# Performance work log

Measured on AMD Instinct MI355X. Metric: run time of the kernel, lower is better.

The kernel has to match this reference:

```python
import jax, jax.numpy as jnp
import numpy as np
from jax import lax

N, E, D, L = 10000, 320000, 128, 5
ATOM_V, BOND_V, WHID, CHID, P = 128, 16, 64, 20, 10
BN_EPS = 1e-5


def setup_inputs() -> dict:
    key = jax.random.key(0)
    it = iter(jax.random.split(key, 40))

    def nrm(shape, fan_in):
        return jax.random.normal(next(it), shape, jnp.float32) / np.sqrt(fan_in).astype(np.float32)

    return {
        "x_feat": jax.random.randint(next(it), (N, 2), 0, ATOM_V),
        "edge_index": jax.random.randint(next(it), (2, E), 0, N),
        "edge_attr": jax.random.randint(next(it), (E, 3), 0, BOND_V),
        "norm_edge_weight": jax.random.uniform(next(it), (E,), jnp.float32),
        "norm_self_loop": jax.random.uniform(next(it), (N,), jnp.float32),
        "atom_emb": nrm((2, ATOM_V, D), 1.0),
        "curv_w1": nrm((D, CHID), D), "curv_b1": jnp.zeros((CHID,), jnp.float32),
        "curv_w2": nrm((CHID, 1), CHID), "curv_b2": jnp.zeros((1,), jnp.float32),
        "fn_w1": nrm((D, CHID), D), "fn_b1": jnp.zeros((CHID,), jnp.float32),
        "fn_w2": nrm((CHID, 1), CHID), "fn_b2": jnp.zeros((1,), jnp.float32),
        "wm_w1": nrm((E, WHID), E), "wm_b1": jnp.zeros((WHID,), jnp.float32),
        "wm_w2": nrm((WHID, WHID), WHID), "wm_b2": jnp.zeros((WHID,), jnp.float32),
        "wm_w3": nrm((WHID, E), WHID), "wm_b3": jnp.zeros((E,), jnp.float32),
        "bond_emb": nrm((L, 3, BOND_V, D), 1.0),
        "conv_w1": nrm((L, D, D), D), "conv_b1": jnp.zeros((L, D), jnp.float32),
        "conv_bn_g": jnp.ones((L, D), jnp.float32), "conv_bn_b": jnp.zeros((L, D), jnp.float32),
        "conv_w2": nrm((L, D, D), D), "conv_b2": jnp.zeros((L, D), jnp.float32),
        "conv_eps": jnp.full((L,), 0.1, jnp.float32),
        "bn_g": jnp.ones((L, D), jnp.float32), "bn_b": jnp.zeros((L, D), jnp.float32),
        "batch": jnp.zeros((N,), jnp.int32),
    }


def _forward(x_feat, edge_index, edge_attr, norm_edge_weight, norm_self_loop,
             atom_emb, curv_w1, curv_b1, curv_w2, curv_b2,
             fn_w1, fn_b1, fn_w2, fn_b2,
             wm_w1, wm_b1, wm_w2, wm_b2, wm_w3, wm_b3,
             bond_emb, conv_w1, conv_b1, conv_bn_g, conv_bn_b, conv_w2, conv_b2,
             conv_eps, bn_g, bn_b):
    relu, sig = jax.nn.relu, jax.nn.sigmoid
    src, dst = edge_index[0], edge_index[1]

    # AtomEncoder: sum of per-column embeddings -> [N, D]
    x = atom_emb[0][x_feat[:, 0]] + atom_emb[1][x_feat[:, 1]]

    # CurvatureMLP: sigmoid(MLP(x)) -> kappa [N, 1]
    kappa = sig(relu(x @ curv_w1 + curv_b1) @ curv_w2 + curv_b2)

    # WeightMLP over 1-D edge-feature-sum vector (single sample of dim E)
    ea = edge_attr.sum(axis=1).astype(jnp.float32)  # [E]
    w = relu(ea @ wm_w1 + wm_b1)
    w = relu(w @ wm_w2 + wm_b2)
    weights = sig(w @ wm_w3 + wm_b3)  # [E]

    # curvature terms: scatter_add at SRC (as in original compute_gamma*)
    seg = lambda v: jax.ops.segment_sum(v, src, num_segments=N)
    f = sig(relu(x @ fn_w1 + fn_b1) @ fn_w2 + fn_b2)[:, 0]  # [N]
    fd = f[dst] - f[src]
    gamma = 0.5 * seg(weights * fd * fd)              # [N]
    delta_f = seg(weights * fd)                       # [N]
    delta_gamma = seg(weights * (gamma[dst] - gamma[src]))
    gfd = 0.5 * seg(weights * fd * (delta_f[dst] - delta_f[src]))
    gamma2 = 0.5 * delta_gamma - gfd                  # [N]
    # NOTE: kappa [N,1] * gamma [N] broadcasts to [N,N] (faithful to original)
    curv_loss = jnp.sum(relu(kappa * gamma - gamma2)) - jnp.sum(kappa)

    kap = kappa[:, 0]

    def bn(h, g, b):  # BatchNorm1d in training mode (batch stats, biased var)
        m = h.mean(axis=0)
        v = jnp.var(h, axis=0)
        return g * (h - m) * lax.rsqrt(v + BN_EPS) + b

    h_list = [x]
    for l in range(L):
        k = min(int(N * P * l / 100), 100)  # num vertices to suppress
        if k > 0:
            idx = lax.top_k(kap, k)[1]
            vm = jnp.ones(N, jnp.float32).at[idx].set(0.0)
            mew = jnp.where((vm[src] == 0) | (vm[dst] == 0), 1e-5, 1.0)
        else:
            mew = jnp.ones(E, jnp.float32)
        # BondEncoder for this layer
        ee = (bond_emb[l, 0][edge_attr[:, 0]]
              + bond_emb[l, 1][edge_attr[:, 1]]
              + bond_emb[l, 2][edge_attr[:, 2]])  # [E, D]
        # message: norm2 * norm * relu(x_j + edge_emb); aggregate add at dst
        msg = (mew * norm_edge_weight)[:, None] * relu(h_list[l][src] + ee)
        aggr = jax.ops.segment_sum(msg, dst, num_segments=N)
        h = conv_eps[l] * norm_self_loop[:, None] * h_list[l] + aggr
        # conv MLP: Linear -> BN -> ReLU -> Linear
        h = relu(bn(h @ conv_w1[l] + conv_b1[l], conv_bn_g[l], conv_bn_b[l])) @ conv_w2[l] + conv_b2[l]
        h = bn(h, bn_g[l], bn_b[l])
        if l < L - 1:  # dropout has ratio 0.0 -> no-op
            h = relu(h)
        h_list.append(h)

    node_rep = h_list[0]
    for h in h_list[1:]:
        node_rep = node_rep + h
    return node_rep, curv_loss


def reference(x_feat, edge_index, edge_attr, norm_edge_weight, norm_self_loop,
              atom_emb, curv_w1, curv_b1, curv_w2, curv_b2,
              fn_w1, fn_b1, fn_w2, fn_b2,
              wm_w1, wm_b1, wm_w2, wm_b2, wm_w3, wm_b3,
              bond_emb, conv_w1, conv_b1, conv_bn_g, conv_bn_b, conv_w2, conv_b2,
              conv_eps, bn_g, bn_b, batch):
    return _forward(x_feat, edge_index, edge_attr, norm_edge_weight, norm_self_loop,
                    atom_emb, curv_w1, curv_b1, curv_w2, curv_b2,
                    fn_w1, fn_b1, fn_w2, fn_b2,
                    wm_w1, wm_b1, wm_w2, wm_b2, wm_w3, wm_b3,
                    bond_emb, conv_w1, conv_b1, conv_bn_g, conv_bn_b, conv_w2, conv_b2,
                    conv_eps, bn_g, bn_b)
```

## Files before the change

kernel.cpp:

```cpp
#include <hip/hip_runtime.h>
#include <hip/hip_bf16.h>
#include <math.h>

#define N_NODES 10000
#define N_EDGES 320000
#define DIM     128
#define NLAYERS 5
#define CHIDN   20
#define BNEPS   1e-5f
#define TOPK    100

__device__ __forceinline__ float sigmoidf_(float x){ return 1.0f/(1.0f + expf(-x)); }

__global__ __launch_bounds__(256) void k_node(
  const int* __restrict__ xf, const float* __restrict__ atom_emb,
  const float* __restrict__ cw1, const float* __restrict__ cb1,
  const float* __restrict__ cw2, const float* __restrict__ cb2,
  const float* __restrict__ fw1, const float* __restrict__ fb1,
  const float* __restrict__ fw2, const float* __restrict__ fb2,
  float* __restrict__ x_out, float* __restrict__ kap, float* __restrict__ fv,
  float* __restrict__ kapparts,
  int* __restrict__ counts, float* __restrict__ gamma, float* __restrict__ delta_f,
  float* __restrict__ dg, float* __restrict__ gfd, double* __restrict__ wh_acc)
{
  __shared__ float scw1[DIM*CHIDN];
  __shared__ float sfw1[DIM*CHIDN];
  __shared__ float sx[4][DIM];
  __shared__ float sred[4][64];
  int tid = threadIdx.x;
  if (tid < 4) {
    int n = blockIdx.x*4 + tid;
    counts[n]=0; gamma[n]=0.f; delta_f[n]=0.f; dg[n]=0.f; gfd[n]=0.f;
  }
  if (blockIdx.x == 0 && tid < 64) wh_acc[tid] = 0.0;
  for (int i=tid;i<DIM*CHIDN;i+=256){ scw1[i]=cw1[i]; sfw1[i]=fw1[i]; }
  int wid = tid>>6, lane = tid&63;
  int n = blockIdx.x*4 + wid;
  const float* e0 = atom_emb;
  const float* e1 = atom_emb + 128*DIM;
  int f0 = xf[n*2+0], f1 = xf[n*2+1];
  float2 a = *(const float2*)(e0 + f0*DIM + lane*2);
  float2 b = *(const float2*)(e1 + f1*DIM + lane*2);
  float2 xv; xv.x = a.x+b.x; xv.y = a.y+b.y;
  *(float2*)(x_out + (size_t)n*DIM + lane*2) = xv;
  sx[wid][lane*2] = xv.x; sx[wid][lane*2+1] = xv.y;
  __syncthreads();
  if (lane < CHIDN) {
    float acc = cb1[lane];
    for (int d=0; d<DIM; ++d) acc = fmaf(sx[wid][d], scw1[d*CHIDN+lane], acc);
    sred[wid][lane] = fmaxf(acc, 0.f) * cw2[lane];
  } else if (lane >= 32 && lane < 32+CHIDN) {
    int hh = lane-32;
    float acc = fb1[hh];
    for (int d=0; d<DIM; ++d) acc = fmaf(sx[wid][d], sfw1[d*CHIDN+hh], acc);
    sred[wid][32+hh] = fmaxf(acc, 0.f) * fw2[hh];
  }
  __syncthreads();
  if (lane == 0) {
    float s = cb2[0];
    for (int h=0;h<CHIDN;++h) s += sred[wid][h];
    float kp = sigmoidf_(s);
    kap[n] = kp;
    sred[wid][62] = kp;
  } else if (lane == 1) {
    float s = fb2[0];
    for (int h=0;h<CHIDN;++h) s += sred[wid][32+h];
    fv[n] = sigmoidf_(s);
  }
  __syncthreads();
  if (tid == 0) {
    kapparts[blockIdx.x] = sred[0][62] + sred[1][62] + sred[2][62] + sred[3][62];
  }
}

__global__ __launch_bounds__(256) void k_edge_pre(
  const int* __restrict__ ei, const int* __restrict__ eattr,
  const float* __restrict__ w1, int* __restrict__ counts, int* __restrict__ rank,
  double* __restrict__ wh_acc)
{
  __shared__ float part_[4][64];
  int tid = threadIdx.x;
  int wid = tid>>6, lane = tid&63;
  int bb = blockIdx.x*4 + wid;
  int e = bb*64 + lane;
  int a0=eattr[e*3], a1=eattr[e*3+1], a2=eattr[e*3+2];
  float ea = (float)(a0+a1+a2);
  int dst = ei[N_EDGES+e];
  rank[e] = atomicAdd(&counts[dst], 1);
  const float4* wrow = (const float4*)(w1 + (size_t)bb*64*64);
  int rsub = lane>>4, c4 = lane&15;
  float4 acc; acc.x=0.f; acc.y=0.f; acc.z=0.f; acc.w=0.f;
  #pragma unroll
  for (int i=0;i<16;++i) {
    float4 v = wrow[(i*4+rsub)*16 + c4];
    float eat = __shfl(ea, i*4+rsub);
    acc.x = fmaf(eat, v.x, acc.x);
    acc.y = fmaf(eat, v.y, acc.y);
    acc.z = fmaf(eat, v.z, acc.z);
    acc.w = fmaf(eat, v.w, acc.w);
  }
  acc.x += __shfl_xor(acc.x, 16); acc.y += __shfl_xor(acc.y, 16);
  acc.z += __shfl_xor(acc.z, 16); acc.w += __shfl_xor(acc.w, 16);
  acc.x += __shfl_xor(acc.x, 32); acc.y += __shfl_xor(acc.y, 32);
  acc.z += __shfl_xor(acc.z, 32); acc.w += __shfl_xor(acc.w, 32);
  if (lane < 16) ((float4*)part_[wid])[c4] = acc;
  __syncthreads();
  if (tid < 64) {
    float s = part_[0][tid]+part_[1][tid]+part_[2][tid]+part_[3][tid];
    atomicAdd(&wh_acc[tid], (double)s);
  }
}

__global__ __launch_bounds__(1024) void k_topk_scan(
  const float* __restrict__ kap, int* __restrict__ mask,
  const int* __restrict__ counts, int* __restrict__ offs)
{
  __shared__ int sbuf[1024];
  __shared__ int hist[256];
  __shared__ unsigned s_prefix;
  __shared__ int s_krem;
  int tid = threadIdx.x;
  if (blockIdx.x == 0) {
    unsigned prefix = 0; int krem = TOPK;
    for (int pass=3; pass>=0; --pass) {
      if (tid<256) hist[tid]=0;
      __syncthreads();
      int shift = pass*8;
      unsigned hi_mask = (pass==3) ? 0u : (0xFFFFFFFFu << (shift+8));
      for (int i=tid;i<N_NODES;i+=1024) {
        unsigned b = __float_as_uint(kap[i]);
        if ((b & hi_mask) == (prefix & hi_mask))
          atomicAdd(&hist[(b>>shift)&255], 1);
      }
      __syncthreads();
      if (tid==0) {
        int c=0; int b=255;
        for (; b>0; --b){ int h=hist[b]; if (c+h >= krem) break; c+=h; }
        s_prefix = prefix | ((unsigned)b << shift);
        s_krem = krem - c;
      }
      __syncthreads();
      prefix = s_prefix; krem = s_krem;
      __syncthreads();
    }
    unsigned thr = prefix;
    const int per = 10;
    int base = tid*per;
    int cnt = 0;
    for (int i=base; i<base+per && i<N_NODES; ++i)
      if (__float_as_uint(kap[i])==thr) cnt++;
    sbuf[tid]=cnt; __syncthreads();
    for (int off=1; off<1024; off<<=1){
      int t = (tid>=off)? sbuf[tid-off] : 0;
      __syncthreads();
      sbuf[tid] += t;
      __syncthreads();
    }
    int taken = sbuf[tid] - cnt;
    for (int i=base; i<base+per && i<N_NODES; ++i) {
      unsigned b = __float_as_uint(kap[i]);
      int sel;
      if (b > thr) sel = 1;
      else if (b == thr) { sel = (taken < krem) ? 1 : 0; taken++; }
      else sel = 0;
      mask[i] = sel;
    }
  } else {
    int run = 0;
    for (int chunk=0; chunk<10; ++chunk) {
      int i = chunk*1024 + tid;
      int v = (i<N_NODES)? counts[i] : 0;
      sbuf[tid]=v; __syncthreads();
      for (int off=1; off<1024; off<<=1){
        int t = (tid>=off)? sbuf[tid-off]:0;
        __syncthreads();
        sbuf[tid]+=t;
        __syncthreads();
      }
      if (i<N_NODES) offs[i+1] = run + sbuf[tid];
      run += sbuf[1023];
      __syncthreads();
    }
    if (tid==0) offs[0]=0;
  }
}

__global__ __launch_bounds__(256) void k_weights_csr(
  const double* __restrict__ wh_acc, const float* __restrict__ wb1,
  const float* __restrict__ wm2, const float* __restrict__ wb2,
  const float* __restrict__ w3, const float* __restrict__ wb3,
  const int* __restrict__ ei, const int* __restrict__ eattr,
  const float* __restrict__ nev, const float* __restrict__ fv,
  const int* __restrict__ mask, const int* __restrict__ offs,
  const int* __restrict__ rank,
  float* __restrict__ weights, float* __restrict__ gamma, float* __restrict__ delta_f,
  int4* __restrict__ csr)
{
  __shared__ float h1[64], h2[64];
  int tid = threadIdx.x;
  if (tid < 64) h1[tid] = fmaxf((float)wh_acc[tid] + wb1[tid], 0.f);
  __syncthreads();
  if (tid < 64) {
    float a = wb2[tid];
    for (int k=0;k<64;++k) a = fmaf(h1[k], wm2[k*64+tid], a);
    h2[tid] = fmaxf(a, 0.f);
  }
  __syncthreads();
  int e = blockIdx.x*256 + tid;
  float ws = wb3[e];
  #pragma unroll 16
  for (int h=0; h<64; ++h) ws = fmaf(h2[h], w3[(size_t)h*N_EDGES + e], ws);
  float wt = sigmoidf_(ws);
  weights[e] = wt;
  int s = ei[e], d = ei[N_EDGES + e];
  float fd = fv[d] - fv[s];
  atomicAdd(&gamma[s], 0.5f*wt*fd*fd);
  atomicAdd(&delta_f[s], wt*fd);
  int a0 = eattr[e*3], a1 = eattr[e*3+1], a2 = eattr[e*3+2];
  float ew = nev[e];
  float mew = (mask[s] | mask[d]) ? 1e-5f : 1.0f;
  int4 rec;
  rec.x = s;
  rec.y = a0 | (a1<<8) | (a2<<16);
  rec.z = __float_as_int(ew);
  rec.w = __float_as_int(mew*ew);
  csr[offs[d] + rank[e]] = rec;
}

__global__ __launch_bounds__(256) void k_edge2(
  const int* __restrict__ ei, const float* __restrict__ weights,
  const float* __restrict__ fv, const float* __restrict__ gamma,
  const float* __restrict__ delta_f,
  float* __restrict__ dg, float* __restrict__ gfd)
{
  int e = blockIdx.x*256 + threadIdx.x;
  int s = ei[e], d = ei[N_EDGES+e];
  float wt = weights[e];
  atomicAdd(&dg[s], wt*(gamma[d]-gamma[s]));
  float fd = fv[d]-fv[s];
  atomicAdd(&gfd[s], wt*fd*(delta_f[d]-delta_f[s]));
}

__global__ __launch_bounds__(256) void k_loss(
  const float* __restrict__ kap, const float* __restrict__ gamma,
  const float* __restrict__ dg, const float* __restrict__ gfd,
  double* __restrict__ lossparts)
{
  __shared__ float skap[1250];
  __shared__ double dred[256];
  int tid = threadIdx.x;
  int i0 = blockIdx.y*1250;
  for (int i=tid;i<1250;i+=256) skap[i]=kap[i0+i];
  __syncthreads();
  int lane = tid & 63, part = tid >> 6;
  int j = blockIdx.x*64 + lane;
  float g=0.f, g2=0.f;
  bool valid = j < N_NODES;
  if (valid){ g = gamma[j]; g2 = 0.5f*(dg[j]-gfd[j]); }
  float sum = 0.f;
  if (valid) {
    int a = part*313, b = a+313; if (b>1250) b=1250;
    for (int i=a;i<b;++i) sum += fmaxf(fmaf(skap[i], g, -g2), 0.f);
  }
  dred[tid] = (double)sum;
  __syncthreads();
  for (int off=128; off>0; off>>=1){
    if (tid<off) dred[tid]+=dred[tid+off];
    __syncthreads();
  }
  if (tid==0) lossparts[blockIdx.y*157 + blockIdx.x] = dred[0];
}

__global__ __launch_bounds__(256) void k_aggr(
  const float* __restrict__ hsrc, const double* __restrict__ statsPrev,
  const float* __restrict__ gPrev, const float* __restrict__ bPrev,
  const int4* __restrict__ csr, const int* __restrict__ offs,
  const float* __restrict__ bond_l, const float* __restrict__ nsl,
  const float* __restrict__ conv_eps, int l, int useW1,
  float* __restrict__ outP, double* __restrict__ stats_l)
{
  __shared__ float tab[3*16*DIM];
  __shared__ float s_sc[DIM], s_sh[DIM];
  __shared__ int4 srec[4][64];
  int tid = threadIdx.x;
  for (int i=tid; i<3*16*DIM; i+=256) tab[i] = bond_l[i];
  bool bn = (statsPrev != nullptr);
  if (bn && tid < DIM) {
    double m = statsPrev[tid] * (1.0/N_NODES);
    double v = statsPrev[DIM+tid] * (1.0/N_NODES) - m*m;
    float inv = (float)(1.0/sqrt(v + (double)BNEPS));
    float sc = gPrev[tid]*inv;
    s_sc[tid]=sc; s_sh[tid]=bPrev[tid]-(float)m*sc;
  }
  if (blockIdx.x == 0) {
    for (int i=tid; i<512; i+=256) stats_l[i] = 0.0;
  }
  __syncthreads();
  int wid = tid>>6, lane = tid&63;
  int n = blockIdx.x*4 + wid;
  float scx=1.f, scy=1.f, shx=0.f, shy=0.f;
  if (bn){ scx=s_sc[lane*2]; scy=s_sc[lane*2+1]; shx=s_sh[lane*2]; shy=s_sh[lane*2+1]; }
  float2 h0 = *(const float2*)(hsrc + (size_t)n*DIM + lane*2);
  if (bn){ h0.x = fmaxf(fmaf(h0.x,scx,shx),0.f); h0.y = fmaxf(fmaf(h0.y,scy,shy),0.f); }
  float c = conv_eps[l] * nsl[n];
  float ax = c*h0.x, ay = c*h0.y;
  int beg = offs[n], end = offs[n+1];
  for (int j0=beg; j0<end; j0+=64) {
    int m = end - j0; if (m>64) m=64;
    if (lane < m) srec[wid][lane] = csr[j0+lane];
    #pragma unroll 4
    for (int t=0;t<m;++t) {
      int4 r = srec[wid][t];
      float wt = __int_as_float(useW1 ? r.w : r.z);
      float2 hs = *(const float2*)(hsrc + (size_t)r.x*DIM + lane*2);
      if (bn){ hs.x = fmaxf(fmaf(hs.x,scx,shx),0.f); hs.y = fmaxf(fmaf(hs.y,scy,shy),0.f); }
      int a0 = r.y&255, a1=(r.y>>8)&255, a2=(r.y>>16)&255;
      float2 e0 = *(const float2*)(tab + a0*DIM + lane*2);
      float2 e1 = *(const float2*)(tab + 16*DIM + a1*DIM + lane*2);
      float2 e2 = *(const float2*)(tab + 32*DIM + a2*DIM + lane*2);
      float vx = hs.x + e0.x + e1.x + e2.x;
      float vy = hs.y + e0.y + e1.y + e2.y;
      ax = fmaf(wt, fmaxf(vx,0.f), ax);
      ay = fmaf(wt, fmaxf(vy,0.f), ay);
    }
  }
  float2 o; o.x=ax; o.y=ay;
  *(float2*)(outP + (size_t)n*DIM + lane*2) = o;
}

__global__ __launch_bounds__(256) void k_gemm(
  const float* __restrict__ A, const float* __restrict__ W,
  const float* __restrict__ bias, float* __restrict__ Out,
  const double* __restrict__ statsIn, const float* __restrict__ gin, const float* __restrict__ bin,
  double* __restrict__ statsOut, int useBnIn)
{
  __shared__ __align__(16) float As[DIM*68];
  __shared__ __align__(16) float Ws[DIM*64];
  __shared__ float s_scale[DIM], s_shift[DIM];
  int tid = threadIdx.x;
  int r0 = blockIdx.x*64, c0 = blockIdx.y*64;
  if (useBnIn) {
    if (tid < DIM) {
      double m = statsIn[tid] * (1.0/N_NODES);
      double v = statsIn[DIM+tid] * (1.0/N_NODES) - m*m;
      float inv = (float)(1.0 / sqrt(v + (double)BNEPS));
      float sc = gin[tid]*inv;
      s_scale[tid] = sc;
      s_shift[tid] = bin[tid] - (float)m*sc;
    }
    __syncthreads();
  }
  for (int i=tid; i<2048; i+=256) {
    int k = i>>4, c4 = i&15;
    *(float4*)(&Ws[k*64 + c4*4]) = *(const float4*)(W + k*DIM + c0 + c4*4);
  }
  for (int i=tid; i<2048; i+=256) {
    int r = i&63, k4 = i>>6;
    int row = r0 + r;
    float4 v;
    if (row < N_NODES) v = *(const float4*)(A + (size_t)row*DIM + k4*4);
    else { v.x=0.f;v.y=0.f;v.z=0.f;v.w=0.f; }
    if (useBnIn) {
      int k = k4*4;
      v.x = fmaxf(fmaf(v.x, s_scale[k+0], s_shift[k+0]), 0.f);
      v.y = fmaxf(fmaf(v.y, s_scale[k+1], s_shift[k+1]), 0.f);
      v.z = fmaxf(fmaf(v.z, s_scale[k+2], s_shift[k+2]), 0.f);
      v.w = fmaxf(fmaf(v.w, s_scale[k+3], s_shift[k+3]), 0.f);
    }
    As[(k4*4+0)*68 + r] = v.x;
    As[(k4*4+1)*68 + r] = v.y;
    As[(k4*4+2)*68 + r] = v.z;
    As[(k4*4+3)*68 + r] = v.w;
  }
  __syncthreads();
  int tc = tid & 15, tr = tid >> 4;
  float acc[4][4];
  #pragma unroll
  for (int i=0;i<4;++i){ acc[i][0]=0.f; acc[i][1]=0.f; acc[i][2]=0.f; acc[i][3]=0.f; }
  #pragma unroll 4
  for (int k=0;k<DIM;++k) {
    float4 a4 = *(const float4*)(&As[k*68 + tr*4]);
    float4 w4 = *(const float4*)(&Ws[k*64 + tc*4]);
    acc[0][0]=fmaf(a4.x,w4.x,acc[0][0]); acc[0][1]=fmaf(a4.x,w4.y,acc[0][1]);
    acc[0][2]=fmaf(a4.x,w4.z,acc[0][2]); acc[0][3]=fmaf(a4.x,w4.w,acc[0][3]);
    acc[1][0]=fmaf(a4.y,w4.x,acc[1][0]); acc[1][1]=fmaf(a4.y,w4.y,acc[1][1]);
    acc[1][2]=fmaf(a4.y,w4.z,acc[1][2]); acc[1][3]=fmaf(a4.y,w4.w,acc[1][3]);
    acc[2][0]=fmaf(a4.z,w4.x,acc[2][0]); acc[2][1]=fmaf(a4.z,w4.y,acc[2][1]);
    acc[2][2]=fmaf(a4.z,w4.z,acc[2][2]); acc[2][3]=fmaf(a4.z,w4.w,acc[2][3]);
    acc[3][0]=fmaf(a4.w,w4.x,acc[3][0]); acc[3][1]=fmaf(a4.w,w4.y,acc[3][1]);
    acc[3][2]=fmaf(a4.w,w4.z,acc[3][2]); acc[3][3]=fmaf(a4.w,w4.w,acc[3][3]);
  }
  __syncthreads();
  float4 b4 = *(const float4*)(bias + c0 + tc*4);
  float ss[4]={0.f,0.f,0.f,0.f}, qq[4]={0.f,0.f,0.f,0.f};
  #pragma unroll
  for (int i=0;i<4;++i) {
    int row = r0 + tr*4 + i;
    if (row < N_NODES) {
      float o0=acc[i][0]+b4.x, o1=acc[i][1]+b4.y, o2=acc[i][2]+b4.z, o3=acc[i][3]+b4.w;
      float4 ov; ov.x=o0; ov.y=o1; ov.z=o2; ov.w=o3;
      *(float4*)(Out + (size_t)row*DIM + c0 + tc*4) = ov;
      ss[0]+=o0; ss[1]+=o1; ss[2]+=o2; ss[3]+=o3;
      qq[0]+=o0*o0; qq[1]+=o1*o1; qq[2]+=o2*o2; qq[3]+=o3*o3;
    }
  }
  float* rs = Ws;
  float* rq = Ws + 1024;
  #pragma unroll
  for (int j=0;j<4;++j){ rs[tr*64 + tc*4+j]=ss[j]; rq[tr*64 + tc*4+j]=qq[j]; }
  __syncthreads();
  if (tid < 64) {
    float s=0.f, q=0.f;
    #pragma unroll
    for (int t=0;t<16;++t){ s += rs[t*64+tid]; q += rq[t*64+tid]; }
    atomicAdd(&statsOut[c0+tid],       (double)s);
    atomicAdd(&statsOut[DIM+c0+tid],   (double)q);
  }
}

__global__ __launch_bounds__(256) void k_final(
  const float* __restrict__ x,
  const float* __restrict__ t0, const float* __restrict__ t1, const float* __restrict__ t2,
  const float* __restrict__ t3, const float* __restrict__ t4,
  const double* __restrict__ stats, const float* __restrict__ bn_g, const float* __restrict__ bn_b,
  const double* __restrict__ lossparts, const float* __restrict__ kapparts,
  float* __restrict__ out)
{
  int tid = threadIdx.x;
  if (blockIdx.x == 0) {
    __shared__ double red[256];
    double acc = 0.0;
    for (int i=tid; i<1256; i+=256) acc += lossparts[i];
    for (int i=tid; i<2500; i+=256) acc -= (double)kapparts[i];
    red[tid] = acc;
    __syncthreads();
    for (int off=128; off>0; off>>=1){
      if (tid<off) red[tid]+=red[tid+off];
      __syncthreads();
    }
    if (tid==0) out[N_NODES*DIM] = (float)red[0];
    return;
  }
  __shared__ float sc[5][DIM], sh[5][DIM];
  if (tid < DIM) {
    for (int l=0;l<5;++l) {
      const double* st = stats + (size_t)l*512 + 256;
      double m = st[tid]*(1.0/N_NODES);
      double v = st[DIM+tid]*(1.0/N_NODES) - m*m;
      float inv = (float)(1.0/sqrt(v + (double)BNEPS));
      float s = bn_g[l*DIM+tid]*inv;
      sc[l][tid]=s; sh[l][tid]=bn_b[l*DIM+tid]-(float)m*s;
    }
  }
  __syncthreads();
  const float* ts[5] = {t0,t1,t2,t3,t4};
  int total = N_NODES*32;
  int stride = (gridDim.x-1)*256;
  for (int i = (blockIdx.x-1)*256 + tid; i < total; i += stride) {
    int c = (i & 31)*4;
    float4 a = ((const float4*)x)[i];
    #pragma unroll
    for (int l=0;l<5;++l) {
      float4 v = ((const float4*)ts[l])[i];
      v.x = fmaf(v.x, sc[l][c+0], sh[l][c+0]);
      v.y = fmaf(v.y, sc[l][c+1], sh[l][c+1]);
      v.z = fmaf(v.z, sc[l][c+2], sh[l][c+2]);
      v.w = fmaf(v.w, sc[l][c+3], sh[l][c+3]);
      if (l < 4) { v.x=fmaxf(v.x,0.f); v.y=fmaxf(v.y,0.f); v.z=fmaxf(v.z,0.f); v.w=fmaxf(v.w,0.f); }
      a.x+=v.x; a.y+=v.y; a.z+=v.z; a.w+=v.w;
    }
    ((float4*)out)[i] = a;
  }
}

extern "C" void kernel_launch(void* const* d_in, const int* in_sizes, int n_in,
                              void* d_out, int out_size, void* d_ws, size_t ws_size,
                              hipStream_t stream)
{
  const int*   x_feat   = (const int*)d_in[0];
  const int*   eidx     = (const int*)d_in[1];
  const int*   eattr    = (const int*)d_in[2];
  const float* nev      = (const float*)d_in[3];
  const float* nsl      = (const float*)d_in[4];
  const float* atom_emb = (const float*)d_in[5];
  const float* cw1 = (const float*)d_in[6];
  const float* cb1 = (const float*)d_in[7];
  const float* cw2 = (const float*)d_in[8];
  const float* cb2 = (const float*)d_in[9];
  const float* fw1 = (const float*)d_in[10];
  const float* fb1 = (const float*)d_in[11];
  const float* fw2 = (const float*)d_in[12];
  const float* fb2 = (const float*)d_in[13];
  const float* wm1 = (const float*)d_in[14];
  const float* wb1 = (const float*)d_in[15];
  const float* wm2 = (const float*)d_in[16];
  const float* wb2 = (const float*)d_in[17];
  const float* wm3 = (const float*)d_in[18];
  const float* wb3 = (const float*)d_in[19];
  const float* bond = (const float*)d_in[20];
  const float* conv_w1 = (const float*)d_in[21];
  const float* conv_b1 = (const float*)d_in[22];
  const float* conv_bn_g = (const float*)d_in[23];
  const float* conv_bn_b = (const float*)d_in[24];
  const float* conv_w2 = (const float*)d_in[25];
  const float* conv_b2 = (const float*)d_in[26];
  const float* conv_eps = (const float*)d_in[27];
  const float* bn_g = (const float*)d_in[28];
  const float* bn_b = (const float*)d_in[29];
  float* out = (float*)d_out;

  char* ws = (char*)d_ws;
  size_t off = 0;
  auto alloc = [&](size_t bytes)->char* {
    char* p = ws + off;
    off += (bytes + 255) & ~(size_t)255;
    return p;
  };
  float* hA       = (float*)alloc((size_t)N_NODES*DIM*4);
  float* bufP     = (float*)alloc((size_t)N_NODES*DIM*4);
  float* bufQ     = (float*)alloc((size_t)N_NODES*DIM*4);
  float* t2b[NLAYERS];
  for (int l=0;l<NLAYERS;++l) t2b[l] = (float*)alloc((size_t)N_NODES*DIM*4);
  int4*  csr      = (int4*)alloc((size_t)N_EDGES*16);
  float* weights  = (float*)alloc((size_t)N_EDGES*4);
  int*   rank     = (int*)alloc((size_t)N_EDGES*4);
  int*   counts   = (int*)alloc((size_t)N_NODES*4);
  int*   offs     = (int*)alloc((size_t)(N_NODES+1)*4);
  float* kap      = (float*)alloc((size_t)N_NODES*4);
  float* fv       = (float*)alloc((size_t)N_NODES*4);
  float* gamma    = (float*)alloc((size_t)N_NODES*4);
  float* delta_f  = (float*)alloc((size_t)N_NODES*4);
  float* dg       = (float*)alloc((size_t)N_NODES*4);
  float* gfd      = (float*)alloc((size_t)N_NODES*4);
  int*   mask     = (int*)alloc((size_t)N_NODES*4);
  double* wh_acc  = (double*)alloc(64*8);
  float* kapparts = (float*)alloc(2500*4);
  double* lossparts = (double*)alloc(1256*8);
  double* stats   = (double*)alloc((size_t)NLAYERS*512*8);

  k_node<<<N_NODES/4, 256, 0, stream>>>(x_feat, atom_emb, cw1,cb1,cw2,cb2, fw1,fb1,fw2,fb2,
                                        hA, kap, fv, kapparts,
                                        counts, gamma, delta_f, dg, gfd, wh_acc);
  k_edge_pre<<<N_EDGES/256, 256, 0, stream>>>(eidx, eattr, wm1, counts, rank, wh_acc);
  k_topk_scan<<<2, 1024, 0, stream>>>(kap, mask, counts, offs);
  k_weights_csr<<<N_EDGES/256, 256, 0, stream>>>(wh_acc, wb1, wm2, wb2, wm3, wb3,
                                                 eidx, eattr, nev, fv, mask, offs, rank,
                                                 weights, gamma, delta_f, csr);
  k_edge2<<<N_EDGES/256, 256, 0, stream>>>(eidx, weights, fv, gamma, delta_f, dg, gfd);
  k_loss<<<dim3((N_NODES+63)/64, 8), 256, 0, stream>>>(kap, gamma, dg, gfd, lossparts);

  for (int l=0; l<NLAYERS; ++l) {
    double* stats_l = stats + (size_t)l*512;
    const float* hsrc = (l==0) ? hA : t2b[l-1];
    const double* statsPrev = (l==0) ? nullptr : (stats + (size_t)(l-1)*512 + 256);
    const float* gPrev = bn_g + (size_t)(l>0?l-1:0)*DIM;
    const float* bPrev = bn_b + (size_t)(l>0?l-1:0)*DIM;
    k_aggr<<<N_NODES/4, 256, 0, stream>>>(hsrc, statsPrev, gPrev, bPrev, csr, offs,
                                          bond + (size_t)l*3*16*DIM, nsl, conv_eps, l,
                                          (l>0)?1:0, bufP, stats_l);
    k_gemm<<<dim3((N_NODES+63)/64, 2), 256, 0, stream>>>(bufP, conv_w1 + (size_t)l*DIM*DIM,
                conv_b1 + l*DIM, bufQ,
                (const double*)nullptr, (const float*)nullptr, (const float*)nullptr,
                stats_l, 0);
    k_gemm<<<dim3((N_NODES+63)/64, 2), 256, 0, stream>>>(bufQ, conv_w2 + (size_t)l*DIM*DIM,
                conv_b2 + l*DIM, t2b[l],
                stats_l, conv_bn_g + l*DIM, conv_bn_b + l*DIM,
                stats_l + 256, 1);
  }
  k_final<<<1025, 256, 0, stream>>>(hA, t2b[0], t2b[1], t2b[2], t2b[3], t2b[4],
                                    stats, bn_g, bn_b, lossparts, kapparts, out);
}
```

Before: 724.3 us.

## Vectorize edge kernels, use wave-shuffle scan, shrink GEMM row tile

Several independent changes. The CSR offset scan now uses wavefront shuffle prefix sums instead of a barrier-heavy shared-memory scan. The edge weight/CSR kernel and the second edge kernel each process four edges per thread with float4/int4 loads. The aggregation inner loop unroll goes from 4 to 8. The GEMM row tile is halved to 32 rows so more blocks run on the many CUs, at the cost of less reuse of the loaded weight tile per block.

```diff
diff --git a/kernel.cpp b/kernel.cpp
--- a/kernel.cpp
+++ b/kernel.cpp
@@ -166,19 +166,27 @@
       mask[i] = sel;
     }
   } else {
+    __shared__ int wsum[16];
+    int lane = tid & 63, w = tid >> 6;
     int run = 0;
     for (int chunk=0; chunk<10; ++chunk) {
       int i = chunk*1024 + tid;
       int v = (i<N_NODES)? counts[i] : 0;
-      sbuf[tid]=v; __syncthreads();
-      for (int off=1; off<1024; off<<=1){
-        int t = (tid>=off)? sbuf[tid-off]:0;
-        __syncthreads();
-        sbuf[tid]+=t;
-        __syncthreads();
+      int x = v;
+      #pragma unroll
+      for (int o=1;o<64;o<<=1){ int t=__shfl_up(x,o); if(lane>=o) x+=t; }
+      if (lane==63) wsum[w]=x;
+      __syncthreads();
+      if (w==0 && lane<16){
+        int y=wsum[lane];
+        #pragma unroll
+        for (int o=1;o<16;o<<=1){ int t=__shfl_up(y,o); if(lane>=o) y+=t; }
+        wsum[lane]=y;
       }
-      if (i<N_NODES) offs[i+1] = run + sbuf[tid];
-      run += sbuf[1023];
+      __syncthreads();
+      int incl = x + ((w>0)? wsum[w-1] : 0);
+      if (i<N_NODES) offs[i+1] = run + incl;
+      run += wsum[15];
       __syncthreads();
     }
     if (tid==0) offs[0]=0;
@@ -206,25 +214,52 @@
     h2[tid] = fmaxf(a, 0.f);
   }
   __syncthreads();
-  int e = blockIdx.x*256 + tid;
-  float ws = wb3[e];
-  #pragma unroll 16
-  for (int h=0; h<64; ++h) ws = fmaf(h2[h], w3[(size_t)h*N_EDGES + e], ws);
-  float wt = sigmoidf_(ws);
-  weights[e] = wt;
-  int s = ei[e], d = ei[N_EDGES + e];
-  float fd = fv[d] - fv[s];
-  atomicAdd(&gamma[s], 0.5f*wt*fd*fd);
-  atomicAdd(&delta_f[s], wt*fd);
-  int a0 = eattr[e*3], a1 = eattr[e*3+1], a2 = eattr[e*3+2];
-  float ew = nev[e];
-  float mew = (mask[s] | mask[d]) ? 1e-5f : 1.0f;
-  int4 rec;
-  rec.x = s;
-  rec.y = a0 | (a1<<8) | (a2<<16);
-  rec.z = __float_as_int(ew);
-  rec.w = __float_as_int(mew*ew);
-  csr[offs[d] + rank[e]] = rec;
+  int e4 = (blockIdx.x*256 + tid)*4;
+  if (e4 >= N_EDGES) return;
+  const float4* w3v = (const float4*)w3;
+  int ecol = e4 >> 2;
+  float4 ws = *(const float4*)(wb3 + e4);
+  #pragma unroll 8
+  for (int h=0; h<64; ++h) {
+    float hv = h2[h];
+    float4 v = w3v[(size_t)h*(N_EDGES/4) + ecol];
+    ws.x = fmaf(hv, v.x, ws.x);
+    ws.y = fmaf(hv, v.y, ws.y);
+    ws.z = fmaf(hv, v.z, ws.z);
+    ws.w = fmaf(hv, v.w, ws.w);
+  }
+  float4 wt4;
+  wt4.x = sigmoidf_(ws.x); wt4.y = sigmoidf_(ws.y);
+  wt4.z = sigmoidf_(ws.z); wt4.w = sigmoidf_(ws.w);
+  *(float4*)(weights + e4) = wt4;
+  int4 s4 = *(const int4*)(ei + e4);
+  int4 d4 = *(const int4*)(ei + N_EDGES + e4);
+  float4 nv = *(const float4*)(nev + e4);
+  int4 r4 = *(const int4*)(rank + e4);
+  int4 ea0 = *(const int4*)(eattr + (size_t)e4*3);
+  int4 ea1 = *(const int4*)(eattr + (size_t)e4*3 + 4);
+  int4 ea2 = *(const int4*)(eattr + (size_t)e4*3 + 8);
+  int at[12] = {ea0.x,ea0.y,ea0.z,ea0.w, ea1.x,ea1.y,ea1.z,ea1.w, ea2.x,ea2.y,ea2.z,ea2.w};
+  int ss[4] = {s4.x,s4.y,s4.z,s4.w};
+  int dd[4] = {d4.x,d4.y,d4.z,d4.w};
+  float wts[4] = {wt4.x,wt4.y,wt4.z,wt4.w};
+  float nvs[4] = {nv.x,nv.y,nv.z,nv.w};
+  int rr[4] = {r4.x,r4.y,r4.z,r4.w};
+  #pragma unroll
+  for (int i=0;i<4;++i) {
+    int s = ss[i], d = dd[i];
+    float wt = wts[i];
+    float fd = fv[d] - fv[s];
+    atomicAdd(&gamma[s], 0.5f*wt*fd*fd);
+    atomicAdd(&delta_f[s], wt*fd);
+    float mew = (mask[s] | mask[d]) ? 1e-5f : 1.0f;
+    int4 rec;
+    rec.x = s;
+    rec.y = at[i*3+0] | (at[i*3+1]<<8) | (at[i*3+2]<<16);
+    rec.z = __float_as_int(nvs[i]);
+    rec.w = __float_as_int(mew*nvs[i]);
+    csr[offs[d] + rr[i]] = rec;
+  }
 }
 
 __global__ __launch_bounds__(256) void k_edge2(
@@ -233,12 +268,22 @@
   const float* __restrict__ delta_f,
   float* __restrict__ dg, float* __restrict__ gfd)
 {
-  int e = blockIdx.x*256 + threadIdx.x;
-  int s = ei[e], d = ei[N_EDGES+e];
-  float wt = weights[e];
-  atomicAdd(&dg[s], wt*(gamma[d]-gamma[s]));
-  float fd = fv[d]-fv[s];
-  atomicAdd(&gfd[s], wt*fd*(delta_f[d]-delta_f[s]));
+  int e4 = (blockIdx.x*256 + threadIdx.x)*4;
+  if (e4 >= N_EDGES) return;
+  int4 s4 = *(const int4*)(ei + e4);
+  int4 d4 = *(const int4*)(ei + N_EDGES + e4);
+  float4 wt4 = *(const float4*)(weights + e4);
+  int ss[4] = {s4.x,s4.y,s4.z,s4.w};
+  int dd[4] = {d4.x,d4.y,d4.z,d4.w};
+  float wts[4] = {wt4.x,wt4.y,wt4.z,wt4.w};
+  #pragma unroll
+  for (int i=0;i<4;++i) {
+    int s = ss[i], d = dd[i];
+    float wt = wts[i];
+    atomicAdd(&dg[s], wt*(gamma[d]-gamma[s]));
+    float fd = fv[d]-fv[s];
+    atomicAdd(&gfd[s], wt*fd*(delta_f[d]-delta_f[s]));
+  }
 }
 
 __global__ __launch_bounds__(256) void k_loss(
@@ -308,7 +353,7 @@
   for (int j0=beg; j0<end; j0+=64) {
     int m = end - j0; if (m>64) m=64;
     if (lane < m) srec[wid][lane] = csr[j0+lane];
-    #pragma unroll 4
+    #pragma unroll 8
     for (int t=0;t<m;++t) {
       int4 r = srec[wid][t];
       float wt = __int_as_float(useW1 ? r.w : r.z);
@@ -334,11 +379,11 @@
   const double* __restrict__ statsIn, const float* __restrict__ gin, const float* __restrict__ bin,
   double* __restrict__ statsOut, int useBnIn)
 {
-  __shared__ __align__(16) float As[DIM*68];
+  __shared__ __align__(16) float As[DIM*36];
   __shared__ __align__(16) float Ws[DIM*64];
   __shared__ float s_scale[DIM], s_shift[DIM];
   int tid = threadIdx.x;
-  int r0 = blockIdx.x*64, c0 = blockIdx.y*64;
+  int r0 = blockIdx.x*32, c0 = blockIdx.y*64;
   if (useBnIn) {
     if (tid < DIM) {
       double m = statsIn[tid] * (1.0/N_NODES);
@@ -354,8 +399,8 @@
     int k = i>>4, c4 = i&15;
     *(float4*)(&Ws[k*64 + c4*4]) = *(const float4*)(W + k*DIM + c0 + c4*4);
   }
-  for (int i=tid; i<2048; i+=256) {
-    int r = i&63, k4 = i>>6;
+  for (int i=tid; i<1024; i+=256) {
+    int r = i&31, k4 = i>>5;
     int row = r0 + r;
     float4 v;
     if (row < N_NODES) v = *(const float4*)(A + (size_t)row*DIM + k4*4);
@@ -367,35 +412,31 @@
       v.z = fmaxf(fmaf(v.z, s_scale[k+2], s_shift[k+2]), 0.f);
       v.w = fmaxf(fmaf(v.w, s_scale[k+3], s_shift[k+3]), 0.f);
     }
-    As[(k4*4+0)*68 + r] = v.x;
-    As[(k4*4+1)*68 + r] = v.y;
-    As[(k4*4+2)*68 + r] = v.z;
-    As[(k4*4+3)*68 + r] = v.w;
+    As[(k4*4+0)*36 + r] = v.x;
+    As[(k4*4+1)*36 + r] = v.y;
+    As[(k4*4+2)*36 + r] = v.z;
+    As[(k4*4+3)*36 + r] = v.w;
   }
   __syncthreads();
   int tc = tid & 15, tr = tid >> 4;
-  float acc[4][4];
+  float acc[2][4];
   #pragma unroll
-  for (int i=0;i<4;++i){ acc[i][0]=0.f; acc[i][1]=0.f; acc[i][2]=0.f; acc[i][3]=0.f; }
-  #pragma unroll 4
+  for (int i=0;i<2;++i){ acc[i][0]=0.f; acc[i][1]=0.f; acc[i][2]=0.f; acc[i][3]=0.f; }
+  #pragma unroll 8
   for (int k=0;k<DIM;++k) {
-    float4 a4 = *(const float4*)(&As[k*68 + tr*4]);
+    float2 a2 = *(const float2*)(&As[k*36 + tr*2]);
     float4 w4 = *(const float4*)(&Ws[k*64 + tc*4]);
-    acc[0][0]=fmaf(a4.x,w4.x,acc[0][0]); acc[0][1]=fmaf(a4.x,w4.y,acc[0][1]);
-    acc[0][2]=fmaf(a4.x,w4.z,acc[0][2]); acc[0][3]=fmaf(a4.x,w4.w,acc[0][3]);
-    acc[1][0]=fmaf(a4.y,w4.x,acc[1][0]); acc[1][1]=fmaf(a4.y,w4.y,acc[1][1]);
-    acc[1][2]=fmaf(a4.y,w4.z,acc[1][2]); acc[1][3]=fmaf(a4.y,w4.w,acc[1][3]);
-    acc[2][0]=fmaf(a4.z,w4.x,acc[2][0]); acc[2][1]=fmaf(a4.z,w4.y,acc[2][1]);
-    acc[2][2]=fmaf(a4.z,w4.z,acc[2][2]); acc[2][3]=fmaf(a4.z,w4.w,acc[2][3]);
-    acc[3][0]=fmaf(a4.w,w4.x,acc[3][0]); acc[3][1]=fmaf(a4.w,w4.y,acc[3][1]);
-    acc[3][2]=fmaf(a4.w,w4.z,acc[3][2]); acc[3][3]=fmaf(a4.w,w4.w,acc[3][3]);
+    acc[0][0]=fmaf(a2.x,w4.x,acc[0][0]); acc[0][1]=fmaf(a2.x,w4.y,acc[0][1]);
+    acc[0][2]=fmaf(a2.x,w4.z,acc[0][2]); acc[0][3]=fmaf(a2.x,w4.w,acc[0][3]);
+    acc[1][0]=fmaf(a2.y,w4.x,acc[1][0]); acc[1][1]=fmaf(a2.y,w4.y,acc[1][1]);
+    acc[1][2]=fmaf(a2.y,w4.z,acc[1][2]); acc[1][3]=fmaf(a2.y,w4.w,acc[1][3]);
   }
   __syncthreads();
   float4 b4 = *(const float4*)(bias + c0 + tc*4);
   float ss[4]={0.f,0.f,0.f,0.f}, qq[4]={0.f,0.f,0.f,0.f};
   #pragma unroll
-  for (int i=0;i<4;++i) {
-    int row = r0 + tr*4 + i;
+  for (int i=0;i<2;++i) {
+    int row = r0 + tr*2 + i;
     if (row < N_NODES) {
       float o0=acc[i][0]+b4.x, o1=acc[i][1]+b4.y, o2=acc[i][2]+b4.z, o3=acc[i][3]+b4.w;
       float4 ov; ov.x=o0; ov.y=o1; ov.z=o2; ov.w=o3;
@@ -543,10 +584,10 @@
                                         counts, gamma, delta_f, dg, gfd, wh_acc);
   k_edge_pre<<<N_EDGES/256, 256, 0, stream>>>(eidx, eattr, wm1, counts, rank, wh_acc);
   k_topk_scan<<<2, 1024, 0, stream>>>(kap, mask, counts, offs);
-  k_weights_csr<<<N_EDGES/256, 256, 0, stream>>>(wh_acc, wb1, wm2, wb2, wm3, wb3,
+  k_weights_csr<<<(N_EDGES/4 + 255)/256, 256, 0, stream>>>(wh_acc, wb1, wm2, wb2, wm3, wb3,
                                                  eidx, eattr, nev, fv, mask, offs, rank,
                                                  weights, gamma, delta_f, csr);
-  k_edge2<<<N_EDGES/256, 256, 0, stream>>>(eidx, weights, fv, gamma, delta_f, dg, gfd);
+  k_edge2<<<(N_EDGES/4 + 255)/256, 256, 0, stream>>>(eidx, weights, fv, gamma, delta_f, dg, gfd);
   k_loss<<<dim3((N_NODES+63)/64, 8), 256, 0, stream>>>(kap, gamma, dg, gfd, lossparts);
 
   for (int l=0; l<NLAYERS; ++l) {
@@ -558,11 +599,11 @@
     k_aggr<<<N_NODES/4, 256, 0, stream>>>(hsrc, statsPrev, gPrev, bPrev, csr, offs,
                                           bond + (size_t)l*3*16*DIM, nsl, conv_eps, l,
                                           (l>0)?1:0, bufP, stats_l);
-    k_gemm<<<dim3((N_NODES+63)/64, 2), 256, 0, stream>>>(bufP, conv_w1 + (size_t)l*DIM*DIM,
+    k_gemm<<<dim3((N_NODES+31)/32, 2), 256, 0, stream>>>(bufP, conv_w1 + (size_t)l*DIM*DIM,
                 conv_b1 + l*DIM, bufQ,
                 (const double*)nullptr, (const float*)nullptr, (const float*)nullptr,
                 stats_l, 0);
-    k_gemm<<<dim3((N_NODES+63)/64, 2), 256, 0, stream>>>(bufQ, conv_w2 + (size_t)l*DIM*DIM,
+    k_gemm<<<dim3((N_NODES+31)/32, 2), 256, 0, stream>>>(bufQ, conv_w2 + (size_t)l*DIM*DIM,
                 conv_b2 + l*DIM, t2b[l],
                 stats_l, conv_bn_g + l*DIM, conv_bn_b + l*DIM,
                 stats_l + 256, 1);
```

Result: slower. 767.9 us (+6.0%).

## Split weights/CSR kernel, vectorize w3 matvec, use wave-shuffle scan, unroll aggregation

Applied to the files above, without the earlier changes.

Splits the fused edge-weight and CSR-build kernel in two, so the 64x320000 w3 matvec runs in its own kernel with float4 loads, each wavefront handling 256 edges and fewer blocks. The offsets prefix scan now uses wavefront shuffles plus a small shared array instead of a 1024-step shared-memory scan with two barriers per step. The aggregation inner loop unroll grows from 4 to 8. The cost is one more kernel launch and an extra round trip of the weights array through global memory.

```diff
diff --git a/kernel.cpp b/kernel.cpp
--- a/kernel.cpp
+++ b/kernel.cpp
@@ -166,35 +166,38 @@
       mask[i] = sel;
     }
   } else {
+    __shared__ int wsum[16];
+    int lane = tid & 63, w = tid >> 6;
     int run = 0;
     for (int chunk=0; chunk<10; ++chunk) {
       int i = chunk*1024 + tid;
       int v = (i<N_NODES)? counts[i] : 0;
-      sbuf[tid]=v; __syncthreads();
-      for (int off=1; off<1024; off<<=1){
-        int t = (tid>=off)? sbuf[tid-off]:0;
-        __syncthreads();
-        sbuf[tid]+=t;
-        __syncthreads();
+      int x = v;
+      #pragma unroll
+      for (int o=1;o<64;o<<=1){ int t=__shfl_up(x,o); if(lane>=o) x+=t; }
+      if (lane==63) wsum[w]=x;
+      __syncthreads();
+      if (w==0 && lane<16){
+        int y=wsum[lane];
+        #pragma unroll
+        for (int o=1;o<16;o<<=1){ int t=__shfl_up(y,o); if(lane>=o) y+=t; }
+        wsum[lane]=y;
       }
-      if (i<N_NODES) offs[i+1] = run + sbuf[tid];
-      run += sbuf[1023];
+      __syncthreads();
+      int incl = x + ((w>0)? wsum[w-1] : 0);
+      if (i<N_NODES) offs[i+1] = run + incl;
+      run += wsum[15];
       __syncthreads();
     }
     if (tid==0) offs[0]=0;
   }
 }
 
-__global__ __launch_bounds__(256) void k_weights_csr(
+__global__ __launch_bounds__(256) void k_weights(
   const double* __restrict__ wh_acc, const float* __restrict__ wb1,
   const float* __restrict__ wm2, const float* __restrict__ wb2,
   const float* __restrict__ w3, const float* __restrict__ wb3,
-  const int* __restrict__ ei, const int* __restrict__ eattr,
-  const float* __restrict__ nev, const float* __restrict__ fv,
-  const int* __restrict__ mask, const int* __restrict__ offs,
-  const int* __restrict__ rank,
-  float* __restrict__ weights, float* __restrict__ gamma, float* __restrict__ delta_f,
-  int4* __restrict__ csr)
+  float* __restrict__ weights)
 {
   __shared__ float h1[64], h2[64];
   int tid = threadIdx.x;
@@ -206,13 +209,38 @@
     h2[tid] = fmaxf(a, 0.f);
   }
   __syncthreads();
-  int e = blockIdx.x*256 + tid;
-  float ws = wb3[e];
+  int wid = tid>>6, lane = tid&63;
+  int base_e = (blockIdx.x*4 + wid)*256;
+  if (base_e >= N_EDGES) return;
+  int col = (base_e>>2) + lane;
+  const float4* w3v = (const float4*)w3;
+  float4 acc = ((const float4*)wb3)[col];
   #pragma unroll 16
-  for (int h=0; h<64; ++h) ws = fmaf(h2[h], w3[(size_t)h*N_EDGES + e], ws);
-  float wt = sigmoidf_(ws);
-  weights[e] = wt;
+  for (int h=0; h<64; ++h) {
+    float hv = h2[h];
+    float4 v = w3v[(size_t)h*(N_EDGES/4) + col];
+    acc.x = fmaf(hv, v.x, acc.x);
+    acc.y = fmaf(hv, v.y, acc.y);
+    acc.z = fmaf(hv, v.z, acc.z);
+    acc.w = fmaf(hv, v.w, acc.w);
+  }
+  float4 wt4;
+  wt4.x = sigmoidf_(acc.x); wt4.y = sigmoidf_(acc.y);
+  wt4.z = sigmoidf_(acc.z); wt4.w = sigmoidf_(acc.w);
+  ((float4*)weights)[col] = wt4;
+}
+
+__global__ __launch_bounds__(256) void k_csr(
+  const int* __restrict__ ei, const int* __restrict__ eattr,
+  const float* __restrict__ nev, const float* __restrict__ weights,
+  const float* __restrict__ fv, const int* __restrict__ mask,
+  const int* __restrict__ offs, const int* __restrict__ rank,
+  float* __restrict__ gamma, float* __restrict__ delta_f,
+  int4* __restrict__ csr)
+{
+  int e = blockIdx.x*256 + threadIdx.x;
   int s = ei[e], d = ei[N_EDGES + e];
+  float wt = weights[e];
   float fd = fv[d] - fv[s];
   atomicAdd(&gamma[s], 0.5f*wt*fd*fd);
   atomicAdd(&delta_f[s], wt*fd);
@@ -308,7 +336,7 @@
   for (int j0=beg; j0<end; j0+=64) {
     int m = end - j0; if (m>64) m=64;
     if (lane < m) srec[wid][lane] = csr[j0+lane];
-    #pragma unroll 4
+    #pragma unroll 8
     for (int t=0;t<m;++t) {
       int4 r = srec[wid][t];
       float wt = __int_as_float(useW1 ? r.w : r.z);
@@ -543,9 +571,9 @@
                                         counts, gamma, delta_f, dg, gfd, wh_acc);
   k_edge_pre<<<N_EDGES/256, 256, 0, stream>>>(eidx, eattr, wm1, counts, rank, wh_acc);
   k_topk_scan<<<2, 1024, 0, stream>>>(kap, mask, counts, offs);
-  k_weights_csr<<<N_EDGES/256, 256, 0, stream>>>(wh_acc, wb1, wm2, wb2, wm3, wb3,
-                                                 eidx, eattr, nev, fv, mask, offs, rank,
-                                                 weights, gamma, delta_f, csr);
+  k_weights<<<313, 256, 0, stream>>>(wh_acc, wb1, wm2, wb2, wm3, wb3, weights);
+  k_csr<<<N_EDGES/256, 256, 0, stream>>>(eidx, eattr, nev, weights, fv, mask, offs, rank,
+                                         gamma, delta_f, csr);
   k_edge2<<<N_EDGES/256, 256, 0, stream>>>(eidx, weights, fv, gamma, delta_f, dg, gfd);
   k_loss<<<dim3((N_NODES+63)/64, 8), 256, 0, stream>>>(kap, gamma, dg, gfd, lossparts);
 
```

After: 752.8 us. 3.9% more time.
